# Optimization experiments

Hardware: AMD Instinct MI355X
Metric: run time of the kernel (lower is better)

Reference implementation:

```python
import jax, jax.numpy as jnp
import numpy as np

N_EMBD = 1024
HEAD_SIZE = 64
B, T = 4, 4096


def setup_inputs() -> dict:
    key = jax.random.key(0)
    kx, kq, kk, kv = jax.random.split(key, 4)
    x = jax.random.normal(kx, (B, T, N_EMBD), dtype=jnp.float32)
    Wq = jax.random.normal(kq, (N_EMBD, HEAD_SIZE), dtype=jnp.float32) * (N_EMBD ** -0.5)
    Wk = jax.random.normal(kk, (N_EMBD, HEAD_SIZE), dtype=jnp.float32) * (N_EMBD ** -0.5)
    Wv = jax.random.normal(kv, (N_EMBD, HEAD_SIZE), dtype=jnp.float32) * (N_EMBD ** -0.5)
    return {"x": x, "Wq": Wq, "Wk": Wk, "Wv": Wv}


def reference(x, Wq, Wk, Wv):
    # x: [B, T, C]; projections: [B, T, H]
    Bv, Tv, C = x.shape
    q = jnp.einsum('btc,ch->bth', x, Wq)
    k = jnp.einsum('btc,ch->bth', x, Wk)
    v = jnp.einsum('btc,ch->bth', x, Wv)
    # NOTE: original scales by C**-0.5 where C = n_embd (not head_size)
    scale = C ** -0.5
    wei = jnp.einsum('bth,bsh->bts', q, k) * scale  # [B, T, T]
    causal = jnp.tril(jnp.ones((Tv, Tv), dtype=bool))
    wei = jnp.where(causal[None, :, :], wei, -jnp.inf)
    wei = jax.nn.softmax(wei, axis=-1)
    # dropout p=0.0 (eval) -> identity
    out = jnp.einsum('bts,bsh->bth', wei, v)  # [B, T, H]
    return out
```

## Files before the change

### kernel.cpp

```cpp
#include <hip/hip_runtime.h>
#include <math.h>

#define Tt 4096
#define Cc 1024
#define Hh 64

typedef __attribute__((ext_vector_type(8))) short bf16x8;
typedef __attribute__((ext_vector_type(4))) float f32x4;
typedef unsigned int u32;

__device__ inline unsigned short f2bf(float f) {
    unsigned u = __float_as_uint(f);
    u = (u + 0x7FFFu + ((u >> 16) & 1u)) >> 16;
    return (unsigned short)u;
}

__global__ __launch_bounds__(256) void wt_build(
    const float* __restrict__ Wq, const float* __restrict__ Wk,
    const float* __restrict__ Wv, unsigned short* __restrict__ Wt)
{
    int e = blockIdx.x * 256 + threadIdx.x;
    int k = e & 1023, n = e >> 10;
    float v;
    if (n < 64)       v = Wq[k * 64 + n] * 0.03125f;
    else if (n < 128) v = Wk[k * 64 + (n - 64)];
    else              v = Wv[k * 64 + (n - 128)];
    Wt[n * 1024 + k] = f2bf(v);
}

__global__ __launch_bounds__(256, 2) void qkv_gemm(
    const float* __restrict__ x, const unsigned short* __restrict__ wt,
    unsigned short* __restrict__ qb, unsigned short* __restrict__ kb,
    unsigned short* __restrict__ vt)
{
    __shared__ unsigned short as_[32 * 1024];

    const int t = threadIdx.x, w = t >> 6, lane = t & 63;
    const int col = lane & 15, quad = lane >> 4;
    const int m0 = blockIdx.x * 32;

    {
        const float* xb = x + (long)m0 * Cc;
        float4 vbuf[16];
#pragma unroll
        for (int g = 0; g < 2; ++g) {
#pragma unroll
            for (int s = 0; s < 16; ++s) {
                int row = g * 16 + s;
                vbuf[s] = *(const float4*)&xb[row * 1024 + t * 4];
            }
#pragma unroll
            for (int s = 0; s < 16; ++s) {
                int row = g * 16 + s;
                ushort4 pk = { f2bf(vbuf[s].x), f2bf(vbuf[s].y),
                               f2bf(vbuf[s].z), f2bf(vbuf[s].w) };
                int woff = (t * 4) ^ ((row & 7) << 3);
                *(ushort4*)&as_[row * 1024 + woff] = pk;
            }
        }
    }
    __syncthreads();

    const unsigned short* aB[2];
#pragma unroll
    for (int kc = 0; kc < 2; ++kc)
        aB[kc] = &as_[col * 1024 + ((kc * 32 + quad * 8) ^ ((col & 7) << 3))];

    const unsigned short* pB[3];
#pragma unroll
    for (int nt = 0; nt < 3; ++nt)
        pB[nt] = wt + ((w * 3 + nt) * 16 + col) * 1024 + quad * 8;

    f32x4 acc[2][3];
#pragma unroll
    for (int mt = 0; mt < 2; ++mt)
#pragma unroll
        for (int nt = 0; nt < 3; ++nt) acc[mt][nt] = (f32x4){0.f, 0.f, 0.f, 0.f};

    bf16x8 bfr[2][3][2];
    bf16x8 afr[2][2][2];

#pragma unroll
    for (int nt = 0; nt < 3; ++nt)
#pragma unroll
        for (int kc = 0; kc < 2; ++kc)
            bfr[0][nt][kc] = *(const bf16x8*)(pB[nt] + kc * 32);
#pragma unroll
    for (int mt = 0; mt < 2; ++mt)
#pragma unroll
        for (int kc = 0; kc < 2; ++kc)
            afr[0][mt][kc] = *(const bf16x8*)(aB[kc] + mt * 16 * 1024);

#pragma unroll
    for (int k = 0; k < 16; ++k) {
        const int cur = k & 1, nxt = cur ^ 1;
        if (k < 15) {
            const int ko = (k + 1) * 64;
#pragma unroll
            for (int nt = 0; nt < 3; ++nt)
#pragma unroll
                for (int kc = 0; kc < 2; ++kc)
                    bfr[nxt][nt][kc] = *(const bf16x8*)(pB[nt] + ko + kc * 32);
#pragma unroll
            for (int mt = 0; mt < 2; ++mt)
#pragma unroll
                for (int kc = 0; kc < 2; ++kc)
                    afr[nxt][mt][kc] = *(const bf16x8*)(aB[kc] + mt * 16 * 1024 + ko);
        }
#pragma unroll
        for (int kc = 0; kc < 2; ++kc)
#pragma unroll
            for (int nt = 0; nt < 3; ++nt)
#pragma unroll
                for (int mt = 0; mt < 2; ++mt)
                    acc[mt][nt] = __builtin_amdgcn_mfma_f32_16x16x32_bf16(
                        afr[cur][mt][kc], bfr[cur][nt][kc], acc[mt][nt], 0, 0, 0);
    }

    const long bidx = m0 >> 12;
    const int tbase = m0 & 4095;
#pragma unroll
    for (int mt = 0; mt < 2; ++mt)
#pragma unroll
        for (int nt = 0; nt < 3; ++nt) {
            int ntg = w * 3 + nt;
            int n = ntg * 16 + col;
            int row = m0 + mt * 16 + quad * 4;
            if (ntg < 4) {
#pragma unroll
                for (int reg = 0; reg < 4; ++reg)
                    qb[(long)(row + reg) * Hh + n] = f2bf(acc[mt][nt][reg]);
            } else if (ntg < 8) {
#pragma unroll
                for (int reg = 0; reg < 4; ++reg)
                    kb[(long)(row + reg) * Hh + (n - 64)] = f2bf(acc[mt][nt][reg]);
            } else {
                int h = n - 128;
                ushort4 pk = { f2bf(acc[mt][nt][0]), f2bf(acc[mt][nt][1]),
                               f2bf(acc[mt][nt][2]), f2bf(acc[mt][nt][3]) };
                *(ushort4*)&vt[(bidx * Hh + h) * (long)Tt + tbase + mt * 16 + quad * 4] = pk;
            }
        }
}

#define LDP 56
#define LDO 68

__global__ __launch_bounds__(256) void attn(
    const unsigned short* __restrict__ qg, const unsigned short* __restrict__ kg,
    const unsigned short* __restrict__ vtg,
    float* __restrict__ po, float* __restrict__ pls)
{
    __shared__ __align__(16) char smem[35328];
    float* o_red       = (float*)smem;
    float* lred        = (float*)(smem + 34816);
    unsigned short* pl = (unsigned short*)smem;

    const int p    = blockIdx.x;
    const int qt   = 127 - (p >> 3);
    const int b    = p & 3;
    const int half = (p >> 2) & 1;
    const int tid  = (b << 7) | qt;
    const long qrow0 = (long)b * Tt + qt * 32;
    const int nkt = qt + 1;
    const int n0  = (nkt + 1) >> 1;
    const int cnt = half ? (nkt - n0) : n0;
    const int ust = half ? n0 : 0;

    const int t = threadIdx.x, w = t >> 6, lane = t & 63;
    const int col = lane & 15, quad = lane >> 4;
    const int plbase = w * 4352;

    bf16x8 qf[2][2];
#pragma unroll
    for (int mt = 0; mt < 2; ++mt)
#pragma unroll
        for (int kc = 0; kc < 2; ++kc)
            qf[mt][kc] = *(const bf16x8*)&qg[(qrow0 + mt * 16 + col) * Hh + kc * 32 + quad * 8];

    f32x4 oacc[2][4];
#pragma unroll
    for (int mt = 0; mt < 2; ++mt)
#pragma unroll
        for (int nt = 0; nt < 4; ++nt) oacc[mt][nt] = (f32x4){0.f, 0.f, 0.f, 0.f};
    float lsum[2][4] = {{0.f,0.f,0.f,0.f},{0.f,0.f,0.f,0.f}};

    auto loadK = [&](bf16x8 (&kf)[2][2], int iu_) {
        const long krow0 = (long)b * Tt + (ust + iu_) * 32;
#pragma unroll
        for (int nt = 0; nt < 2; ++nt)
#pragma unroll
            for (int kc = 0; kc < 2; ++kc)
                kf[nt][kc] = *(const bf16x8*)&kg[(krow0 + nt * 16 + col) * Hh + kc * 32 + quad * 8];
    };
    auto loadV = [&](bf16x8 (&vf)[4], int iu_) {
        const int u = ust + iu_;
#pragma unroll
        for (int nt = 0; nt < 4; ++nt)
            vf[nt] = *(const bf16x8*)&vtg[((long)b * Hh + nt * 16 + col) * Tt + u * 32 + quad * 8];
    };
    auto compute = [&](bf16x8 (&kf)[2][2], bf16x8 (&vf)[4], int u) {
        f32x4 s[2][2];
        __builtin_amdgcn_s_setprio(1);
#pragma unroll
        for (int mt = 0; mt < 2; ++mt)
#pragma unroll
            for (int nt = 0; nt < 2; ++nt) {
                s[mt][nt] = (f32x4){0.f, 0.f, 0.f, 0.f};
#pragma unroll
                for (int kc = 0; kc < 2; ++kc)
                    s[mt][nt] = __builtin_amdgcn_mfma_f32_16x16x32_bf16(
                        qf[mt][kc], kf[nt][kc], s[mt][nt], 0, 0, 0);
            }
        __builtin_amdgcn_s_setprio(0);
#pragma unroll
        for (int mt = 0; mt < 2; ++mt)
#pragma unroll
            for (int reg = 0; reg < 4; ++reg) {
                int rloc = mt * 16 + quad * 4 + reg;
                if (u == qt) {
                    if (col > rloc)      s[mt][0][reg] = -INFINITY;
                    if (16 + col > rloc) s[mt][1][reg] = -INFINITY;
                }
                float p0 = __expf(s[mt][0][reg]);
                float p1 = __expf(s[mt][1][reg]);
                lsum[mt][reg] += p0 + p1;
                pl[plbase + rloc * LDP + col]      = f2bf(p0);
                pl[plbase + rloc * LDP + 16 + col] = f2bf(p1);
            }
        bf16x8 af0 = *(const bf16x8*)&pl[plbase + col * LDP + quad * 8];
        bf16x8 af1 = *(const bf16x8*)&pl[plbase + (16 + col) * LDP + quad * 8];
        __builtin_amdgcn_s_setprio(1);
#pragma unroll
        for (int nt = 0; nt < 4; ++nt) {
            oacc[0][nt] = __builtin_amdgcn_mfma_f32_16x16x32_bf16(af0, vf[nt], oacc[0][nt], 0, 0, 0);
            oacc[1][nt] = __builtin_amdgcn_mfma_f32_16x16x32_bf16(af1, vf[nt], oacc[1][nt], 0, 0, 0);
        }
        __builtin_amdgcn_s_setprio(0);
    };

    bf16x8 kA[2][2], vA[4], kB[2][2], vB[4];
    int iu = w;
    if (iu < cnt) { loadK(kA, iu); loadV(vA, iu); }
    while (iu < cnt) {
        int i1 = iu + 4;
        if (i1 < cnt) { loadK(kB, i1); loadV(vB, i1); }
        compute(kA, vA, ust + iu);
        if (i1 >= cnt) break;
        int i2 = i1 + 4;
        if (i2 < cnt) { loadK(kA, i2); loadV(vA, i2); }
        compute(kB, vB, ust + i1);
        iu = i2;
    }

#pragma unroll
    for (int mt = 0; mt < 2; ++mt)
#pragma unroll
        for (int reg = 0; reg < 4; ++reg) {
            float l = lsum[mt][reg];
            l += __shfl_xor(l, 1); l += __shfl_xor(l, 2);
            l += __shfl_xor(l, 4); l += __shfl_xor(l, 8);
            if (col == 0) lred[w * 32 + mt * 16 + quad * 4 + reg] = l;
        }
#pragma unroll
    for (int mt = 0; mt < 2; ++mt)
#pragma unroll
        for (int nt = 0; nt < 4; ++nt)
#pragma unroll
            for (int reg = 0; reg < 4; ++reg)
                o_red[(w * 32 + mt * 16 + quad * 4 + reg) * LDO + nt * 16 + col] = oacc[mt][nt][reg];
    __syncthreads();
    if (t < 32)
        pls[(tid * 2 + half) * 32 + t] = lred[t] + lred[32 + t] + lred[64 + t] + lred[96 + t];
    float* pob = po + ((long)tid * 2 + half) * 2048;
#pragma unroll
    for (int j = 0; j < 8; ++j) {
        int e = t + 256 * j, r = e >> 6, c = e & 63;
        pob[e] = o_red[r * LDO + c] + o_red[(32 + r) * LDO + c]
               + o_red[(64 + r) * LDO + c] + o_red[(96 + r) * LDO + c];
    }
}

__global__ __launch_bounds__(256) void combine(
    const float* __restrict__ po, const float* __restrict__ pls, float* __restrict__ out)
{
    const int g = blockIdx.x;
    const long orow = (((long)(g >> 7)) * Tt + (long)(g & 127) * 32) * Hh;
    const float* p0 = po + (long)g * 2 * 2048;
    const float* p1 = p0 + 2048;
    const float* l0 = pls + g * 2 * 32;
    const float* l1 = l0 + 32;
    const int t = threadIdx.x;
#pragma unroll
    for (int j = 0; j < 8; ++j) {
        int e = t + 256 * j, r = e >> 6;
        out[orow + e] = (p0[e] + p1[e]) / (l0[r] + l1[r]);
    }
}

extern "C" void kernel_launch(void* const* d_in, const int* in_sizes, int n_in,
                              void* d_out, int out_size, void* d_ws, size_t ws_size,
                              hipStream_t stream)
{
    const float* x  = (const float*)d_in[0];
    const float* Wq = (const float*)d_in[1];
    const float* Wk = (const float*)d_in[2];
    const float* Wv = (const float*)d_in[3];
    float* outp = (float*)d_out;

    unsigned short* wt = (unsigned short*)d_ws;
    unsigned short* qb = wt + 196608;
    unsigned short* kb = qb + 1048576;
    unsigned short* vt = kb + 1048576;
    float* po  = (float*)(vt + 1048576);
    float* pls = po + 2097152;

    wt_build<<<dim3(768), dim3(256), 0, stream>>>(Wq, Wk, Wv, wt);
    qkv_gemm<<<dim3(512), dim3(256), 0, stream>>>(x, wt, qb, kb, vt);
    attn<<<dim3(1024), dim3(256), 0, stream>>>(qb, kb, vt, po, pls);
    combine<<<dim3(512), dim3(256), 0, stream>>>(po, pls, outp);
}
```

Baseline: 161.4 us.

## Split attention KV range four ways and pair light/heavy query tiles per block

Each attention block now handles two query tiles, j and 127-j, so causal work is balanced across blocks. For each tile the key range is split into four slices instead of two. The explicit double-buffered K/V register prefetch and setprio hints are removed in favour of a simple loop with pointer increments. The combine kernel now sums four partials, which doubles partial-output traffic and workspace use, and the loads may lose some latency hiding.

```diff
diff --git a/kernel.cpp b/kernel.cpp
--- a/kernel.cpp
+++ b/kernel.cpp
@@ -156,129 +156,117 @@
     float* lred        = (float*)(smem + 34816);
     unsigned short* pl = (unsigned short*)smem;
 
-    const int p    = blockIdx.x;
-    const int qt   = 127 - (p >> 3);
-    const int b    = p & 3;
-    const int half = (p >> 2) & 1;
-    const int tid  = (b << 7) | qt;
-    const long qrow0 = (long)b * Tt + qt * 32;
-    const int nkt = qt + 1;
-    const int n0  = (nkt + 1) >> 1;
-    const int cnt = half ? (nkt - n0) : n0;
-    const int ust = half ? n0 : 0;
+    const int p     = blockIdx.x;
+    const int s_idx = p & 3;
+    const int b     = (p >> 2) & 3;
+    const int j     = p >> 4;
 
     const int t = threadIdx.x, w = t >> 6, lane = t & 63;
     const int col = lane & 15, quad = lane >> 4;
     const int plbase = w * 4352;
 
-    bf16x8 qf[2][2];
-#pragma unroll
-    for (int mt = 0; mt < 2; ++mt)
-#pragma unroll
-        for (int kc = 0; kc < 2; ++kc)
-            qf[mt][kc] = *(const bf16x8*)&qg[(qrow0 + mt * 16 + col) * Hh + kc * 32 + quad * 8];
-
-    f32x4 oacc[2][4];
-#pragma unroll
-    for (int mt = 0; mt < 2; ++mt)
-#pragma unroll
-        for (int nt = 0; nt < 4; ++nt) oacc[mt][nt] = (f32x4){0.f, 0.f, 0.f, 0.f};
-    float lsum[2][4] = {{0.f,0.f,0.f,0.f},{0.f,0.f,0.f,0.f}};
-
-    auto loadK = [&](bf16x8 (&kf)[2][2], int iu_) {
-        const long krow0 = (long)b * Tt + (ust + iu_) * 32;
-#pragma unroll
-        for (int nt = 0; nt < 2; ++nt)
+    auto runPhase = [&](int qt) {
+        const int nkt = qt + 1;
+        const int q4 = nkt >> 2, r4 = nkt & 3;
+        const int start = s_idx * q4 + (s_idx < r4 ? s_idx : r4);
+        const int cnt   = q4 + (s_idx < r4 ? 1 : 0);
+        const int gbase = (((b << 7) | qt) << 2) | s_idx;
+        const long qrow0 = (long)b * Tt + qt * 32;
+
+        bf16x8 qf[2][2];
+#pragma unroll
+        for (int mt = 0; mt < 2; ++mt)
 #pragma unroll
             for (int kc = 0; kc < 2; ++kc)
-                kf[nt][kc] = *(const bf16x8*)&kg[(krow0 + nt * 16 + col) * Hh + kc * 32 + quad * 8];
+                qf[mt][kc] = *(const bf16x8*)&qg[(qrow0 + mt * 16 + col) * Hh + kc * 32 + quad * 8];
+
+        f32x4 oacc[2][4];
+#pragma unroll
+        for (int mt = 0; mt < 2; ++mt)
+#pragma unroll
+            for (int nt = 0; nt < 4; ++nt) oacc[mt][nt] = (f32x4){0.f, 0.f, 0.f, 0.f};
+        float lsum[2][4] = {{0.f,0.f,0.f,0.f},{0.f,0.f,0.f,0.f}};
+
+        const int udiag = qt - start;
+        const unsigned short* kp = kg +
+            (((long)b * Tt + (long)(start + w) * 32 + col) << 6) + quad * 8;
+        const unsigned short* vp = vtg +
+            (((long)b * Hh + col) << 12) + (start + w) * 32 + quad * 8;
+
+        for (int iu = w; iu < cnt; iu += 4, kp += 8192, vp += 128) {
+            bf16x8 kf[2][2];
+#pragma unroll
+            for (int nt = 0; nt < 2; ++nt)
+#pragma unroll
+                for (int kc = 0; kc < 2; ++kc)
+                    kf[nt][kc] = *(const bf16x8*)(kp + nt * 1024 + kc * 32);
+            f32x4 s[2][2];
+#pragma unroll
+            for (int mt = 0; mt < 2; ++mt)
+#pragma unroll
+                for (int nt = 0; nt < 2; ++nt) {
+                    s[mt][nt] = (f32x4){0.f, 0.f, 0.f, 0.f};
+#pragma unroll
+                    for (int kc = 0; kc < 2; ++kc)
+                        s[mt][nt] = __builtin_amdgcn_mfma_f32_16x16x32_bf16(
+                            qf[mt][kc], kf[nt][kc], s[mt][nt], 0, 0, 0);
+                }
+#pragma unroll
+            for (int mt = 0; mt < 2; ++mt)
+#pragma unroll
+                for (int reg = 0; reg < 4; ++reg) {
+                    int rloc = mt * 16 + quad * 4 + reg;
+                    if (iu == udiag) {
+                        if (col > rloc)      s[mt][0][reg] = -INFINITY;
+                        if (16 + col > rloc) s[mt][1][reg] = -INFINITY;
+                    }
+                    float p0 = __expf(s[mt][0][reg]);
+                    float p1 = __expf(s[mt][1][reg]);
+                    lsum[mt][reg] += p0 + p1;
+                    pl[plbase + rloc * LDP + col]      = f2bf(p0);
+                    pl[plbase + rloc * LDP + 16 + col] = f2bf(p1);
+                }
+            bf16x8 af0 = *(const bf16x8*)&pl[plbase + col * LDP + quad * 8];
+            bf16x8 af1 = *(const bf16x8*)&pl[plbase + (16 + col) * LDP + quad * 8];
+#pragma unroll
+            for (int nt = 0; nt < 4; ++nt) {
+                bf16x8 vf = *(const bf16x8*)(vp + nt * 65536);
+                oacc[0][nt] = __builtin_amdgcn_mfma_f32_16x16x32_bf16(af0, vf, oacc[0][nt], 0, 0, 0);
+                oacc[1][nt] = __builtin_amdgcn_mfma_f32_16x16x32_bf16(af1, vf, oacc[1][nt], 0, 0, 0);
+            }
+        }
+
+#pragma unroll
+        for (int mt = 0; mt < 2; ++mt)
+#pragma unroll
+            for (int reg = 0; reg < 4; ++reg) {
+                float l = lsum[mt][reg];
+                l += __shfl_xor(l, 1); l += __shfl_xor(l, 2);
+                l += __shfl_xor(l, 4); l += __shfl_xor(l, 8);
+                if (col == 0) lred[w * 32 + mt * 16 + quad * 4 + reg] = l;
+            }
+#pragma unroll
+        for (int mt = 0; mt < 2; ++mt)
+#pragma unroll
+            for (int nt = 0; nt < 4; ++nt)
+#pragma unroll
+                for (int reg = 0; reg < 4; ++reg)
+                    o_red[(w * 32 + mt * 16 + quad * 4 + reg) * LDO + nt * 16 + col] = oacc[mt][nt][reg];
+        __syncthreads();
+        if (t < 32)
+            pls[gbase * 32 + t] = lred[t] + lred[32 + t] + lred[64 + t] + lred[96 + t];
+        float* pob = po + (long)gbase * 2048;
+#pragma unroll
+        for (int jj = 0; jj < 8; ++jj) {
+            int e = t + 256 * jj, r = e >> 6, c = e & 63;
+            pob[e] = o_red[r * LDO + c] + o_red[(32 + r) * LDO + c]
+                   + o_red[(64 + r) * LDO + c] + o_red[(96 + r) * LDO + c];
+        }
+        __syncthreads();
     };
-    auto loadV = [&](bf16x8 (&vf)[4], int iu_) {
-        const int u = ust + iu_;
-#pragma unroll
-        for (int nt = 0; nt < 4; ++nt)
-            vf[nt] = *(const bf16x8*)&vtg[((long)b * Hh + nt * 16 + col) * Tt + u * 32 + quad * 8];
-    };
-    auto compute = [&](bf16x8 (&kf)[2][2], bf16x8 (&vf)[4], int u) {
-        f32x4 s[2][2];
-        __builtin_amdgcn_s_setprio(1);
-#pragma unroll
-        for (int mt = 0; mt < 2; ++mt)
-#pragma unroll
-            for (int nt = 0; nt < 2; ++nt) {
-                s[mt][nt] = (f32x4){0.f, 0.f, 0.f, 0.f};
-#pragma unroll
-                for (int kc = 0; kc < 2; ++kc)
-                    s[mt][nt] = __builtin_amdgcn_mfma_f32_16x16x32_bf16(
-                        qf[mt][kc], kf[nt][kc], s[mt][nt], 0, 0, 0);
-            }
-        __builtin_amdgcn_s_setprio(0);
-#pragma unroll
-        for (int mt = 0; mt < 2; ++mt)
-#pragma unroll
-            for (int reg = 0; reg < 4; ++reg) {
-                int rloc = mt * 16 + quad * 4 + reg;
-                if (u == qt) {
-                    if (col > rloc)      s[mt][0][reg] = -INFINITY;
-                    if (16 + col > rloc) s[mt][1][reg] = -INFINITY;
-                }
-                float p0 = __expf(s[mt][0][reg]);
-                float p1 = __expf(s[mt][1][reg]);
-                lsum[mt][reg] += p0 + p1;
-                pl[plbase + rloc * LDP + col]      = f2bf(p0);
-                pl[plbase + rloc * LDP + 16 + col] = f2bf(p1);
-            }
-        bf16x8 af0 = *(const bf16x8*)&pl[plbase + col * LDP + quad * 8];
-        bf16x8 af1 = *(const bf16x8*)&pl[plbase + (16 + col) * LDP + quad * 8];
-        __builtin_amdgcn_s_setprio(1);
-#pragma unroll
-        for (int nt = 0; nt < 4; ++nt) {
-            oacc[0][nt] = __builtin_amdgcn_mfma_f32_16x16x32_bf16(af0, vf[nt], oacc[0][nt], 0, 0, 0);
-            oacc[1][nt] = __builtin_amdgcn_mfma_f32_16x16x32_bf16(af1, vf[nt], oacc[1][nt], 0, 0, 0);
-        }
-        __builtin_amdgcn_s_setprio(0);
-    };
-
-    bf16x8 kA[2][2], vA[4], kB[2][2], vB[4];
-    int iu = w;
-    if (iu < cnt) { loadK(kA, iu); loadV(vA, iu); }
-    while (iu < cnt) {
-        int i1 = iu + 4;
-        if (i1 < cnt) { loadK(kB, i1); loadV(vB, i1); }
-        compute(kA, vA, ust + iu);
-        if (i1 >= cnt) break;
-        int i2 = i1 + 4;
-        if (i2 < cnt) { loadK(kA, i2); loadV(vA, i2); }
-        compute(kB, vB, ust + i1);
-        iu = i2;
-    }
-
-#pragma unroll
-    for (int mt = 0; mt < 2; ++mt)
-#pragma unroll
-        for (int reg = 0; reg < 4; ++reg) {
-            float l = lsum[mt][reg];
-            l += __shfl_xor(l, 1); l += __shfl_xor(l, 2);
-            l += __shfl_xor(l, 4); l += __shfl_xor(l, 8);
-            if (col == 0) lred[w * 32 + mt * 16 + quad * 4 + reg] = l;
-        }
-#pragma unroll
-    for (int mt = 0; mt < 2; ++mt)
-#pragma unroll
-        for (int nt = 0; nt < 4; ++nt)
-#pragma unroll
-            for (int reg = 0; reg < 4; ++reg)
-                o_red[(w * 32 + mt * 16 + quad * 4 + reg) * LDO + nt * 16 + col] = oacc[mt][nt][reg];
-    __syncthreads();
-    if (t < 32)
-        pls[(tid * 2 + half) * 32 + t] = lred[t] + lred[32 + t] + lred[64 + t] + lred[96 + t];
-    float* pob = po + ((long)tid * 2 + half) * 2048;
-#pragma unroll
-    for (int j = 0; j < 8; ++j) {
-        int e = t + 256 * j, r = e >> 6, c = e & 63;
-        pob[e] = o_red[r * LDO + c] + o_red[(32 + r) * LDO + c]
-               + o_red[(64 + r) * LDO + c] + o_red[(96 + r) * LDO + c];
-    }
+
+    runPhase(j);
+    runPhase(127 - j);
 }
 
 __global__ __launch_bounds__(256) void combine(
@@ -286,15 +274,14 @@
 {
     const int g = blockIdx.x;
     const long orow = (((long)(g >> 7)) * Tt + (long)(g & 127) * 32) * Hh;
-    const float* p0 = po + (long)g * 2 * 2048;
-    const float* p1 = p0 + 2048;
-    const float* l0 = pls + g * 2 * 32;
-    const float* l1 = l0 + 32;
+    const float* pp = po  + (long)g * 4 * 2048;
+    const float* ll = pls + (long)g * 4 * 32;
     const int t = threadIdx.x;
 #pragma unroll
     for (int j = 0; j < 8; ++j) {
         int e = t + 256 * j, r = e >> 6;
-        out[orow + e] = (p0[e] + p1[e]) / (l0[r] + l1[r]);
+        float l = ll[r] + ll[32 + r] + ll[64 + r] + ll[96 + r];
+        out[orow + e] = (pp[e] + pp[2048 + e] + pp[4096 + e] + pp[6144 + e]) / l;
     }
 }
 
@@ -313,7 +300,7 @@
     unsigned short* kb = qb + 1048576;
     unsigned short* vt = kb + 1048576;
     float* po  = (float*)(vt + 1048576);
-    float* pls = po + 2097152;
+    float* pls = po + 4194304;
 
     wt_build<<<dim3(768), dim3(256), 0, stream>>>(Wq, Wk, Wv, wt);
     qkv_gemm<<<dim3(512), dim3(256), 0, stream>>>(x, wt, qb, kb, vt);
```

Result: slower. 171.1 us (+6.0%).
